# Kernel tuning notes

Measured on AMD Instinct MI355X. Metric: run time of the kernel, lower is better.

## Reference

```python
import jax, jax.numpy as jnp
import numpy as np

B, I, K, C = 4, 512, 512, 64
EPS_LN = 1e-5


def _ln_last2(x):
    # functional layer_norm over the last TWO dims, no affine params
    mu = x.mean(axis=(-2, -1), keepdims=True)
    var = ((x - mu) ** 2).mean(axis=(-2, -1), keepdims=True)
    return (x - mu) / jnp.sqrt(var + EPS_LN)


def setup_inputs() -> dict:
    key = jax.random.key(0)
    k1, k2, k3, k4, k5, k6, k7, k8 = jax.random.split(key, 8)
    V = jax.random.normal(k1, (B, I, C), dtype=jnp.float32)
    Q = jax.random.normal(k2, (B, K, C), dtype=jnp.float32)
    z = jax.random.normal(k3, (B, I, K, C), dtype=jnp.float32)
    z_mask = (jax.random.uniform(k4, (B, I, K)) > 0.3).astype(jnp.float32)
    s = 1.0 / np.sqrt(C)
    W1 = jax.random.normal(k5, (C, C), dtype=jnp.float32) * s
    b1 = jax.random.normal(k6, (C,), dtype=jnp.float32) * 0.01
    W2 = jax.random.normal(k7, (C, C), dtype=jnp.float32) * s
    b2 = jax.random.normal(k8, (C,), dtype=jnp.float32) * 0.01
    return {"V": V, "Q": Q, "z": z, "z_mask": z_mask,
            "W1": W1, "b1": b1, "W2": W2, "b2": b2, "dim": 1}


def reference(V, Q, z, z_mask, W1, b1, W2, b2, dim):
    normalize = True
    # masked exponential normalization along `dim` (per channel c)
    exp_z = jnp.exp(z) * (z_mask[..., None] + 1e-6)          # [b,i,k,c]
    zn = exp_z / exp_z.sum(axis=dim, keepdims=True)
    zn = z_mask[..., None] * zn
    Qa = Q @ W1.T + b1                                       # linear1
    if dim == 1:
        Va = jnp.einsum('bikc,bkc->bic', zn, Qa)
    else:
        Va = jnp.einsum('bikc,bic->bkc', zn, Qa)
    if normalize:
        Va = _ln_last2(Va)
    Vout = V + (Va @ W2.T + b2)                              # linear2 + residual
    if normalize:
        Vout = _ln_last2(Vout)
    return Vout
```

## Files before the change

kernel.cpp:

```cpp
#include <hip/hip_runtime.h>

constexpr int NB = 4;
constexpr int NI = 512;
constexpr int NK = 512;
constexpr int NC = 64;
constexpr float LN_EPS = 1e-5f;

__global__ __launch_bounds__(256) void k_S(const float* __restrict__ z,
                                           const float* __restrict__ zmask,
                                           float* __restrict__ S) {
    int idx = blockIdx.x;
    int ic = idx & 7;  idx >>= 3;
    int kt = idx & 31; int b = idx >> 5;
    int tid = threadIdx.x;
    int kk = tid >> 4;
    int c4 = tid & 15;
    int k = kt * 16 + kk;

    float4 acc = make_float4(0.f, 0.f, 0.f, 0.f);
    for (int ii = 0; ii < NI / 8; ++ii) {
        int i = ic * (NI / 8) + ii;
        size_t row = ((size_t)(b * NI + i) * NK + k) * NC;
        const float4 zv = *(const float4*)(z + row + c4 * 4);
        float m = zmask[(size_t)(b * NI + i) * NK + k] + 1e-6f;
        acc.x += __expf(zv.x) * m;
        acc.y += __expf(zv.y) * m;
        acc.z += __expf(zv.z) * m;
        acc.w += __expf(zv.w) * m;
    }
    float* sp = S + (size_t)(b * NK + k) * NC + c4 * 4;
    atomicAdd(sp + 0, acc.x);
    atomicAdd(sp + 1, acc.y);
    atomicAdd(sp + 2, acc.z);
    atomicAdd(sp + 3, acc.w);
}

__global__ __launch_bounds__(64) void k_R(const float* __restrict__ Q,
                                          const float* __restrict__ W1,
                                          const float* __restrict__ b1,
                                          const float* __restrict__ S,
                                          float* __restrict__ R) {
    int bk = blockIdx.x;
    int c = threadIdx.x;
    __shared__ float q[NC];
    q[c] = Q[(size_t)bk * NC + c];
    __syncthreads();
    const float* w = W1 + c * NC;
    float acc = b1[c];
#pragma unroll
    for (int j = 0; j < NC; ++j) acc += q[j] * w[j];
    R[(size_t)bk * NC + c] = acc / S[(size_t)bk * NC + c];
}

__global__ __launch_bounds__(256) void k_Va(const float* __restrict__ z,
                                            const float* __restrict__ zmask,
                                            const float* __restrict__ R,
                                            float* __restrict__ Va,
                                            float* __restrict__ part1) {
    int bi = blockIdx.x;
    int b = bi >> 9;
    int tid = threadIdx.x;
    int kk = tid >> 4;
    int c4 = tid & 15;

    const float* zrow = z + (size_t)bi * NK * NC;
    const float* mrow = zmask + (size_t)bi * NK;
    const float* Rb = R + (size_t)b * NK * NC;

    float4 acc = make_float4(0.f, 0.f, 0.f, 0.f);
    for (int kb = 0; kb < NK / 16; ++kb) {
        int k = kb * 16 + kk;
        const float4 zv = *(const float4*)(zrow + (size_t)k * NC + c4 * 4);
        const float4 rv = *(const float4*)(Rb + (size_t)k * NC + c4 * 4);
        float zm = mrow[k];
        float m2 = zm * (zm + 1e-6f);
        acc.x += __expf(zv.x) * m2 * rv.x;
        acc.y += __expf(zv.y) * m2 * rv.y;
        acc.z += __expf(zv.z) * m2 * rv.z;
        acc.w += __expf(zv.w) * m2 * rv.w;
    }

    __shared__ float4 part[256];
    part[tid] = acc;
    __syncthreads();
    for (int s = 128; s >= 16; s >>= 1) {
        if (tid < s) {
            float4 o = part[tid + s];
            float4 m = part[tid];
            m.x += o.x; m.y += o.y; m.z += o.z; m.w += o.w;
            part[tid] = m;
        }
        __syncthreads();
    }
    __shared__ float red[32];
    if (tid < 16) {
        float4 v = part[tid];
        *(float4*)(Va + (size_t)bi * NC + tid * 4) = v;
        red[tid]      = v.x + v.y + v.z + v.w;
        red[16 + tid] = v.x * v.x + v.y * v.y + v.z * v.z + v.w * v.w;
    }
    __syncthreads();
    if (tid == 0) {
        float s0 = 0.f, s1 = 0.f;
        for (int t = 0; t < 16; ++t) { s0 += red[t]; s1 += red[16 + t]; }
        part1[bi * 2]     = s0;
        part1[bi * 2 + 1] = s1;
    }
}

__global__ __launch_bounds__(256) void k_red(const float* __restrict__ part,
                                             float* __restrict__ stats) {
    int b = blockIdx.x;
    int tid = threadIdx.x;
    float s0 = 0.f, s1 = 0.f;
    for (int i = tid; i < NI; i += 256) {
        int bi = b * NI + i;
        s0 += part[bi * 2];
        s1 += part[bi * 2 + 1];
    }
    __shared__ float l0[256], l1[256];
    l0[tid] = s0; l1[tid] = s1;
    __syncthreads();
    for (int s = 128; s; s >>= 1) {
        if (tid < s) { l0[tid] += l0[tid + s]; l1[tid] += l1[tid + s]; }
        __syncthreads();
    }
    if (tid == 0) { stats[b * 2] = l0[0]; stats[b * 2 + 1] = l1[0]; }
}

__global__ __launch_bounds__(64) void k_Y(const float* __restrict__ V,
                                          const float* __restrict__ W2,
                                          const float* __restrict__ b2,
                                          const float* __restrict__ Va,
                                          const float* __restrict__ stats1,
                                          float* __restrict__ Y,
                                          float* __restrict__ part2) {
    int bi = blockIdx.x;
    int b = bi >> 9;
    int c = threadIdx.x;
    const float n = (float)(NI * NC);
    float mu = stats1[b * 2] / n;
    float var = stats1[b * 2 + 1] / n - mu * mu;
    float rstd = rsqrtf(var + LN_EPS);

    __shared__ float xn[NC];
    xn[c] = (Va[(size_t)bi * NC + c] - mu) * rstd;
    __syncthreads();

    const float* w = W2 + c * NC;
    float acc = b2[c];
#pragma unroll
    for (int j = 0; j < NC; ++j) acc += xn[j] * w[j];
    float y = V[(size_t)bi * NC + c] + acc;
    Y[(size_t)bi * NC + c] = y;

    float s0 = y, s1 = y * y;
    for (int off = 32; off; off >>= 1) {
        s0 += __shfl_down(s0, off);
        s1 += __shfl_down(s1, off);
    }
    if (c == 0) { part2[bi * 2] = s0; part2[bi * 2 + 1] = s1; }
}

__global__ __launch_bounds__(256) void k_out(const float* __restrict__ Y,
                                             const float* __restrict__ stats2,
                                             float* __restrict__ out) {
    int idx = blockIdx.x * 256 + threadIdx.x;
    int b = idx >> 15;
    const float n = (float)(NI * NC);
    float mu = stats2[b * 2] / n;
    float var = stats2[b * 2 + 1] / n - mu * mu;
    float rstd = rsqrtf(var + LN_EPS);
    out[idx] = (Y[idx] - mu) * rstd;
}

extern "C" void kernel_launch(void* const* d_in, const int* in_sizes, int n_in,
                              void* d_out, int out_size, void* d_ws, size_t ws_size,
                              hipStream_t stream) {
    const float* V  = (const float*)d_in[0];
    const float* Q  = (const float*)d_in[1];
    const float* z  = (const float*)d_in[2];
    const float* zm = (const float*)d_in[3];
    const float* W1 = (const float*)d_in[4];
    const float* b1 = (const float*)d_in[5];
    const float* W2 = (const float*)d_in[6];
    const float* b2 = (const float*)d_in[7];

    float* ws     = (float*)d_ws;
    float* S      = ws;
    float* R      = ws + 131072;
    float* Va     = ws + 262144;
    float* Y      = ws + 393216;
    float* part1  = ws + 524288;
    float* part2  = ws + 528384;
    float* stats1 = ws + 532480;
    float* stats2 = ws + 532488;

    hipMemsetAsync(S, 0, 131072 * sizeof(float), stream);

    k_S  <<<NB * (NK / 16) * 8, 256, 0, stream>>>(z, zm, S);
    k_R  <<<NB * NK,            64,  0, stream>>>(Q, W1, b1, S, R);
    k_Va <<<NB * NI,            256, 0, stream>>>(z, zm, R, Va, part1);
    k_red<<<NB,                 256, 0, stream>>>(part1, stats1);
    k_Y  <<<NB * NI,            64,  0, stream>>>(V, W2, b2, Va, stats1, Y, part2);
    k_red<<<NB,                 256, 0, stream>>>(part2, stats2);
    k_out<<<(NB * NI * NC) / 256, 256, 0, stream>>>(Y, stats2, (float*)d_out);
}
```

Baseline: 438.6 us.

## Process batches sequentially so z slice stays cached between sum and weighting passes

Splits the normalization-sum, R and weighted-accumulation kernels into a per-batch loop so the second read of each batch's z slice can hit the last-level cache instead of HBM. Replaces atomic accumulation into S (and its memset) with per-chunk partial sums written to workspace and reduced in k_R, using 32 i-chunks. Adds unroll pragmas. Trades more kernel launches and partial-sum traffic for halving expected DRAM reads of z.

```diff
diff --git a/kernel.cpp b/kernel.cpp
--- a/kernel.cpp
+++ b/kernel.cpp
@@ -6,20 +6,24 @@
 constexpr int NC = 64;
 constexpr float LN_EPS = 1e-5f;
 
+constexpr int IC = 32;
+constexpr int ILEN = NI / IC;
+
 __global__ __launch_bounds__(256) void k_S(const float* __restrict__ z,
                                            const float* __restrict__ zmask,
-                                           float* __restrict__ S) {
+                                           float* __restrict__ Spart, int b) {
     int idx = blockIdx.x;
-    int ic = idx & 7;  idx >>= 3;
-    int kt = idx & 31; int b = idx >> 5;
+    int ic = idx & (IC - 1);
+    int kt = idx >> 5;
     int tid = threadIdx.x;
     int kk = tid >> 4;
     int c4 = tid & 15;
     int k = kt * 16 + kk;
 
     float4 acc = make_float4(0.f, 0.f, 0.f, 0.f);
-    for (int ii = 0; ii < NI / 8; ++ii) {
-        int i = ic * (NI / 8) + ii;
+#pragma unroll 4
+    for (int ii = 0; ii < ILEN; ++ii) {
+        int i = ic * ILEN + ii;
         size_t row = ((size_t)(b * NI + i) * NK + k) * NC;
         const float4 zv = *(const float4*)(z + row + c4 * 4);
         float m = zmask[(size_t)(b * NI + i) * NK + k] + 1e-6f;
@@ -28,37 +32,37 @@
         acc.z += __expf(zv.z) * m;
         acc.w += __expf(zv.w) * m;
     }
-    float* sp = S + (size_t)(b * NK + k) * NC + c4 * 4;
-    atomicAdd(sp + 0, acc.x);
-    atomicAdd(sp + 1, acc.y);
-    atomicAdd(sp + 2, acc.z);
-    atomicAdd(sp + 3, acc.w);
+    *(float4*)(Spart + (size_t)ic * (NK * NC) + (size_t)k * NC + c4 * 4) = acc;
 }
 
 __global__ __launch_bounds__(64) void k_R(const float* __restrict__ Q,
                                           const float* __restrict__ W1,
                                           const float* __restrict__ b1,
-                                          const float* __restrict__ S,
-                                          float* __restrict__ R) {
-    int bk = blockIdx.x;
+                                          const float* __restrict__ Spart,
+                                          float* __restrict__ R, int b) {
+    int k = blockIdx.x;
     int c = threadIdx.x;
     __shared__ float q[NC];
-    q[c] = Q[(size_t)bk * NC + c];
+    q[c] = Q[((size_t)(b * NK) + k) * NC + c];
     __syncthreads();
     const float* w = W1 + c * NC;
     float acc = b1[c];
 #pragma unroll
     for (int j = 0; j < NC; ++j) acc += q[j] * w[j];
-    R[(size_t)bk * NC + c] = acc / S[(size_t)bk * NC + c];
+    float s = 0.f;
+#pragma unroll
+    for (int ic = 0; ic < IC; ++ic)
+        s += Spart[(size_t)ic * (NK * NC) + (size_t)k * NC + c];
+    R[((size_t)(b * NK) + k) * NC + c] = acc / s;
 }
 
 __global__ __launch_bounds__(256) void k_Va(const float* __restrict__ z,
                                             const float* __restrict__ zmask,
                                             const float* __restrict__ R,
                                             float* __restrict__ Va,
-                                            float* __restrict__ part1) {
-    int bi = blockIdx.x;
-    int b = bi >> 9;
+                                            float* __restrict__ part1, int b) {
+    int i = blockIdx.x;
+    int bi = b * NI + i;
     int tid = threadIdx.x;
     int kk = tid >> 4;
     int c4 = tid & 15;
@@ -68,6 +72,7 @@
     const float* Rb = R + (size_t)b * NK * NC;
 
     float4 acc = make_float4(0.f, 0.f, 0.f, 0.f);
+#pragma unroll 2
     for (int kb = 0; kb < NK / 16; ++kb) {
         int k = kb * 16 + kk;
         const float4 zv = *(const float4*)(zrow + (size_t)k * NC + c4 * 4);
@@ -187,20 +192,20 @@
     const float* b2 = (const float*)d_in[7];
 
     float* ws     = (float*)d_ws;
-    float* S      = ws;
-    float* R      = ws + 131072;
-    float* Va     = ws + 262144;
-    float* Y      = ws + 393216;
-    float* part1  = ws + 524288;
-    float* part2  = ws + 528384;
-    float* stats1 = ws + 532480;
-    float* stats2 = ws + 532488;
-
-    hipMemsetAsync(S, 0, 131072 * sizeof(float), stream);
-
-    k_S  <<<NB * (NK / 16) * 8, 256, 0, stream>>>(z, zm, S);
-    k_R  <<<NB * NK,            64,  0, stream>>>(Q, W1, b1, S, R);
-    k_Va <<<NB * NI,            256, 0, stream>>>(z, zm, R, Va, part1);
+    float* Spart  = ws;
+    float* R      = ws + 1048576;
+    float* Va     = ws + 1179648;
+    float* Y      = ws + 1310720;
+    float* part1  = ws + 1441792;
+    float* part2  = ws + 1445888;
+    float* stats1 = ws + 1449984;
+    float* stats2 = ws + 1449992;
+
+    for (int b = 0; b < NB; ++b) {
+        k_S <<<(NK / 16) * IC, 256, 0, stream>>>(z, zm, Spart, b);
+        k_R <<<NK,             64,  0, stream>>>(Q, W1, b1, Spart, R, b);
+        k_Va<<<NI,             256, 0, stream>>>(z, zm, R, Va, part1, b);
+    }
     k_red<<<NB,                 256, 0, stream>>>(part1, stats1);
     k_Y  <<<NB * NI,            64,  0, stream>>>(V, W2, b2, Va, stats1, Y, part2);
     k_red<<<NB,                 256, 0, stream>>>(part2, stats2);
```

Result: slower. 457.5 us (+4.3%).

## Replace atomic column sums with partial buffers and unroll z streaming loops

Applied to the files above, without the earlier changes.

The column-sum kernel now splits I into 16 chunks and writes per-chunk partial sums to a workspace buffer instead of using atomicAdd. The R kernel reduces those partials, which also removes the memset. Both z-streaming kernels are unrolled with four independent accumulators so more loads are in flight. This uses more workspace and adds extra partial-sum reads in k_R.

```diff
diff --git a/kernel.cpp b/kernel.cpp
--- a/kernel.cpp
+++ b/kernel.cpp
@@ -6,39 +6,57 @@
 constexpr int NC = 64;
 constexpr float LN_EPS = 1e-5f;
 
+constexpr int IC = 16;
+constexpr int ILEN = NI / IC;
+constexpr size_t SP_STRIDE = (size_t)NB * NK * NC;
+
 __global__ __launch_bounds__(256) void k_S(const float* __restrict__ z,
                                            const float* __restrict__ zmask,
-                                           float* __restrict__ S) {
+                                           float* __restrict__ Spart) {
     int idx = blockIdx.x;
-    int ic = idx & 7;  idx >>= 3;
+    int ic = idx & (IC - 1); idx >>= 4;
     int kt = idx & 31; int b = idx >> 5;
     int tid = threadIdx.x;
     int kk = tid >> 4;
     int c4 = tid & 15;
     int k = kt * 16 + kk;
 
-    float4 acc = make_float4(0.f, 0.f, 0.f, 0.f);
-    for (int ii = 0; ii < NI / 8; ++ii) {
-        int i = ic * (NI / 8) + ii;
-        size_t row = ((size_t)(b * NI + i) * NK + k) * NC;
-        const float4 zv = *(const float4*)(z + row + c4 * 4);
-        float m = zmask[(size_t)(b * NI + i) * NK + k] + 1e-6f;
-        acc.x += __expf(zv.x) * m;
-        acc.y += __expf(zv.y) * m;
-        acc.z += __expf(zv.z) * m;
-        acc.w += __expf(zv.w) * m;
-    }
-    float* sp = S + (size_t)(b * NK + k) * NC + c4 * 4;
-    atomicAdd(sp + 0, acc.x);
-    atomicAdd(sp + 1, acc.y);
-    atomicAdd(sp + 2, acc.z);
-    atomicAdd(sp + 3, acc.w);
+    float4 a0 = make_float4(0.f, 0.f, 0.f, 0.f);
+    float4 a1 = a0, a2 = a0, a3 = a0;
+
+    int i0 = ic * ILEN;
+#pragma unroll 2
+    for (int ii = 0; ii < ILEN; ii += 4) {
+        size_t base = (size_t)(b * NI + i0 + ii) * NK + k;
+        const float4 z0 = *(const float4*)(z + (base         ) * NC + c4 * 4);
+        const float4 z1 = *(const float4*)(z + (base +     NK) * NC + c4 * 4);
+        const float4 z2 = *(const float4*)(z + (base + 2 * NK) * NC + c4 * 4);
+        const float4 z3 = *(const float4*)(z + (base + 3 * NK) * NC + c4 * 4);
+        float m0 = zmask[base         ] + 1e-6f;
+        float m1 = zmask[base +     NK] + 1e-6f;
+        float m2 = zmask[base + 2 * NK] + 1e-6f;
+        float m3 = zmask[base + 3 * NK] + 1e-6f;
+        a0.x += __expf(z0.x) * m0; a0.y += __expf(z0.y) * m0;
+        a0.z += __expf(z0.z) * m0; a0.w += __expf(z0.w) * m0;
+        a1.x += __expf(z1.x) * m1; a1.y += __expf(z1.y) * m1;
+        a1.z += __expf(z1.z) * m1; a1.w += __expf(z1.w) * m1;
+        a2.x += __expf(z2.x) * m2; a2.y += __expf(z2.y) * m2;
+        a2.z += __expf(z2.z) * m2; a2.w += __expf(z2.w) * m2;
+        a3.x += __expf(z3.x) * m3; a3.y += __expf(z3.y) * m3;
+        a3.z += __expf(z3.z) * m3; a3.w += __expf(z3.w) * m3;
+    }
+    float4 acc;
+    acc.x = (a0.x + a1.x) + (a2.x + a3.x);
+    acc.y = (a0.y + a1.y) + (a2.y + a3.y);
+    acc.z = (a0.z + a1.z) + (a2.z + a3.z);
+    acc.w = (a0.w + a1.w) + (a2.w + a3.w);
+    *(float4*)(Spart + (size_t)ic * SP_STRIDE + ((size_t)(b * NK) + k) * NC + c4 * 4) = acc;
 }
 
 __global__ __launch_bounds__(64) void k_R(const float* __restrict__ Q,
                                           const float* __restrict__ W1,
                                           const float* __restrict__ b1,
-                                          const float* __restrict__ S,
+                                          const float* __restrict__ Spart,
                                           float* __restrict__ R) {
     int bk = blockIdx.x;
     int c = threadIdx.x;
@@ -49,7 +67,11 @@
     float acc = b1[c];
 #pragma unroll
     for (int j = 0; j < NC; ++j) acc += q[j] * w[j];
-    R[(size_t)bk * NC + c] = acc / S[(size_t)bk * NC + c];
+    float s = 0.f;
+#pragma unroll
+    for (int ic = 0; ic < IC; ++ic)
+        s += Spart[(size_t)ic * SP_STRIDE + (size_t)bk * NC + c];
+    R[(size_t)bk * NC + c] = acc / s;
 }
 
 __global__ __launch_bounds__(256) void k_Va(const float* __restrict__ z,
@@ -63,22 +85,41 @@
     int kk = tid >> 4;
     int c4 = tid & 15;
 
-    const float* zrow = z + (size_t)bi * NK * NC;
+    const float* zrow = z + (size_t)bi * NK * NC + c4 * 4;
     const float* mrow = zmask + (size_t)bi * NK;
-    const float* Rb = R + (size_t)b * NK * NC;
-
-    float4 acc = make_float4(0.f, 0.f, 0.f, 0.f);
-    for (int kb = 0; kb < NK / 16; ++kb) {
-        int k = kb * 16 + kk;
-        const float4 zv = *(const float4*)(zrow + (size_t)k * NC + c4 * 4);
-        const float4 rv = *(const float4*)(Rb + (size_t)k * NC + c4 * 4);
-        float zm = mrow[k];
-        float m2 = zm * (zm + 1e-6f);
-        acc.x += __expf(zv.x) * m2 * rv.x;
-        acc.y += __expf(zv.y) * m2 * rv.y;
-        acc.z += __expf(zv.z) * m2 * rv.z;
-        acc.w += __expf(zv.w) * m2 * rv.w;
-    }
+    const float* Rb = R + (size_t)b * NK * NC + c4 * 4;
+
+    float4 a0 = make_float4(0.f, 0.f, 0.f, 0.f);
+    float4 a1 = a0, a2 = a0, a3 = a0;
+#pragma unroll 2
+    for (int kb = 0; kb < NK / 64; ++kb) {
+        int k0 = kb * 64 + kk;
+        const float4 z0 = *(const float4*)(zrow + (size_t)(k0     ) * NC);
+        const float4 z1 = *(const float4*)(zrow + (size_t)(k0 + 16) * NC);
+        const float4 z2 = *(const float4*)(zrow + (size_t)(k0 + 32) * NC);
+        const float4 z3 = *(const float4*)(zrow + (size_t)(k0 + 48) * NC);
+        const float4 r0 = *(const float4*)(Rb + (size_t)(k0     ) * NC);
+        const float4 r1 = *(const float4*)(Rb + (size_t)(k0 + 16) * NC);
+        const float4 r2 = *(const float4*)(Rb + (size_t)(k0 + 32) * NC);
+        const float4 r3 = *(const float4*)(Rb + (size_t)(k0 + 48) * NC);
+        float w0 = mrow[k0];      w0 = w0 * (w0 + 1e-6f);
+        float w1 = mrow[k0 + 16]; w1 = w1 * (w1 + 1e-6f);
+        float w2 = mrow[k0 + 32]; w2 = w2 * (w2 + 1e-6f);
+        float w3 = mrow[k0 + 48]; w3 = w3 * (w3 + 1e-6f);
+        a0.x += __expf(z0.x) * w0 * r0.x; a0.y += __expf(z0.y) * w0 * r0.y;
+        a0.z += __expf(z0.z) * w0 * r0.z; a0.w += __expf(z0.w) * w0 * r0.w;
+        a1.x += __expf(z1.x) * w1 * r1.x; a1.y += __expf(z1.y) * w1 * r1.y;
+        a1.z += __expf(z1.z) * w1 * r1.z; a1.w += __expf(z1.w) * w1 * r1.w;
+        a2.x += __expf(z2.x) * w2 * r2.x; a2.y += __expf(z2.y) * w2 * r2.y;
+        a2.z += __expf(z2.z) * w2 * r2.z; a2.w += __expf(z2.w) * w2 * r2.w;
+        a3.x += __expf(z3.x) * w3 * r3.x; a3.y += __expf(z3.y) * w3 * r3.y;
+        a3.z += __expf(z3.z) * w3 * r3.z; a3.w += __expf(z3.w) * w3 * r3.w;
+    }
+    float4 acc;
+    acc.x = (a0.x + a1.x) + (a2.x + a3.x);
+    acc.y = (a0.y + a1.y) + (a2.y + a3.y);
+    acc.z = (a0.z + a1.z) + (a2.z + a3.z);
+    acc.w = (a0.w + a1.w) + (a2.w + a3.w);
 
     __shared__ float4 part[256];
     part[tid] = acc;
@@ -187,22 +228,20 @@
     const float* b2 = (const float*)d_in[7];
 
     float* ws     = (float*)d_ws;
-    float* S      = ws;
-    float* R      = ws + 131072;
-    float* Va     = ws + 262144;
-    float* Y      = ws + 393216;
-    float* part1  = ws + 524288;
-    float* part2  = ws + 528384;
-    float* stats1 = ws + 532480;
-    float* stats2 = ws + 532488;
-
-    hipMemsetAsync(S, 0, 131072 * sizeof(float), stream);
-
-    k_S  <<<NB * (NK / 16) * 8, 256, 0, stream>>>(z, zm, S);
-    k_R  <<<NB * NK,            64,  0, stream>>>(Q, W1, b1, S, R);
-    k_Va <<<NB * NI,            256, 0, stream>>>(z, zm, R, Va, part1);
-    k_red<<<NB,                 256, 0, stream>>>(part1, stats1);
-    k_Y  <<<NB * NI,            64,  0, stream>>>(V, W2, b2, Va, stats1, Y, part2);
-    k_red<<<NB,                 256, 0, stream>>>(part2, stats2);
+    float* Spart  = ws;
+    float* R      = ws + 2097152;
+    float* Va     = ws + 2228224;
+    float* Y      = ws + 2359296;
+    float* part1  = ws + 2490368;
+    float* part2  = ws + 2494464;
+    float* stats1 = ws + 2498560;
+    float* stats2 = ws + 2498568;
+
+    k_S  <<<NB * (NK / 16) * IC, 256, 0, stream>>>(z, zm, Spart);
+    k_R  <<<NB * NK,             64,  0, stream>>>(Q, W1, b1, Spart, R);
+    k_Va <<<NB * NI,             256, 0, stream>>>(z, zm, R, Va, part1);
+    k_red<<<NB,                  256, 0, stream>>>(part1, stats1);
+    k_Y  <<<NB * NI,             64,  0, stream>>>(V, W2, b2, Va, stats1, Y, part2);
+    k_red<<<NB,                  256, 0, stream>>>(part2, stats2);
     k_out<<<(NB * NI * NC) / 256, 256, 0, stream>>>(Y, stats2, (float*)d_out);
 }
```

Result: no change. 440.6 us (+0.5%).

## Stream contiguous z slabs per block and replace atomics with partial sums

Applied to the files above, without the earlier changes.

k_S now has each 512-thread block stream whole contiguous [K,C] slabs of z for a strided set of i rows. It keeps 16 float4 accumulators per thread and writes per-block partial S slabs instead of issuing atomicAdds, and the memset goes away. k_R sums the 64 partial slabs per (b,k,c). k_Va processes four full i-rows per block with the mask staged in LDS and uses a wave-shuffle reduction in place of the shared-memory tree. The aim is fully coalesced, contiguous reads of the 256MB z tensor and no atomic contention. The cost is a 32MB partial buffer, extra reads in k_R and higher register pressure in k_S.

```diff
diff --git a/kernel.cpp b/kernel.cpp
--- a/kernel.cpp
+++ b/kernel.cpp
@@ -6,41 +6,57 @@
 constexpr int NC = 64;
 constexpr float LN_EPS = 1e-5f;
 
-__global__ __launch_bounds__(256) void k_S(const float* __restrict__ z,
+
+constexpr int SBLK = 64;
+constexpr int SLAB = NK * NC;
+constexpr int NSLAB = NB * SBLK;
+
+__global__ __launch_bounds__(512) void k_S(const float* __restrict__ z,
                                            const float* __restrict__ zmask,
-                                           float* __restrict__ S) {
-    int idx = blockIdx.x;
-    int ic = idx & 7;  idx >>= 3;
-    int kt = idx & 31; int b = idx >> 5;
+                                           float* __restrict__ Spart) {
+    int blk = blockIdx.x;
+    int b = blk >> 6;
+    int ic = blk & (SBLK - 1);
     int tid = threadIdx.x;
-    int kk = tid >> 4;
-    int c4 = tid & 15;
-    int k = kt * 16 + kk;
-
-    float4 acc = make_float4(0.f, 0.f, 0.f, 0.f);
-    for (int ii = 0; ii < NI / 8; ++ii) {
-        int i = ic * (NI / 8) + ii;
-        size_t row = ((size_t)(b * NI + i) * NK + k) * NC;
-        const float4 zv = *(const float4*)(z + row + c4 * 4);
-        float m = zmask[(size_t)(b * NI + i) * NK + k] + 1e-6f;
-        acc.x += __expf(zv.x) * m;
-        acc.y += __expf(zv.y) * m;
-        acc.z += __expf(zv.z) * m;
-        acc.w += __expf(zv.w) * m;
-    }
-    float* sp = S + (size_t)(b * NK + k) * NC + c4 * 4;
-    atomicAdd(sp + 0, acc.x);
-    atomicAdd(sp + 1, acc.y);
-    atomicAdd(sp + 2, acc.z);
-    atomicAdd(sp + 3, acc.w);
+    int kg = tid >> 4;
+
+    __shared__ float mlds[NK];
+
+    float4 acc[16];
+#pragma unroll
+    for (int s = 0; s < 16; ++s) acc[s] = make_float4(0.f, 0.f, 0.f, 0.f);
+
+    for (int ii = 0; ii < NI / SBLK; ++ii) {
+        int i = ii * SBLK + ic;
+        const float* zs = z + (size_t)(b * NI + i) * SLAB;
+        const float* mp = zmask + (size_t)(b * NI + i) * NK;
+        __syncthreads();
+        mlds[tid] = mp[tid];
+        __syncthreads();
+#pragma unroll
+        for (int s = 0; s < 16; ++s) {
+            const float4 zv = *(const float4*)(zs + (size_t)(s * 512 + tid) * 4);
+            float w = mlds[s * 32 + kg] + 1e-6f;
+            acc[s].x += __expf(zv.x) * w;
+            acc[s].y += __expf(zv.y) * w;
+            acc[s].z += __expf(zv.z) * w;
+            acc[s].w += __expf(zv.w) * w;
+        }
+    }
+    float* sp = Spart + (size_t)blk * SLAB;
+#pragma unroll
+    for (int s = 0; s < 16; ++s)
+        *(float4*)(sp + (size_t)(s * 512 + tid) * 4) = acc[s];
 }
 
 __global__ __launch_bounds__(64) void k_R(const float* __restrict__ Q,
                                           const float* __restrict__ W1,
                                           const float* __restrict__ b1,
-                                          const float* __restrict__ S,
+                                          const float* __restrict__ Spart,
                                           float* __restrict__ R) {
     int bk = blockIdx.x;
+    int b = bk >> 9;
+    int k = bk & (NK - 1);
     int c = threadIdx.x;
     __shared__ float q[NC];
     q[c] = Q[(size_t)bk * NC + c];
@@ -49,62 +65,80 @@
     float acc = b1[c];
 #pragma unroll
     for (int j = 0; j < NC; ++j) acc += q[j] * w[j];
-    R[(size_t)bk * NC + c] = acc / S[(size_t)bk * NC + c];
-}
-
-__global__ __launch_bounds__(256) void k_Va(const float* __restrict__ z,
+    float s = 0.f;
+#pragma unroll 8
+    for (int j = 0; j < SBLK; ++j)
+        s += Spart[(size_t)((b << 6) + j) * SLAB + (size_t)k * NC + c];
+    R[(size_t)bk * NC + c] = acc / s;
+}
+
+__global__ __launch_bounds__(512) void k_Va(const float* __restrict__ z,
                                             const float* __restrict__ zmask,
                                             const float* __restrict__ R,
                                             float* __restrict__ Va,
                                             float* __restrict__ part1) {
-    int bi = blockIdx.x;
-    int b = bi >> 9;
+    int blk = blockIdx.x;
+    int b = blk >> 7;
+    int ic = blk & 127;
     int tid = threadIdx.x;
-    int kk = tid >> 4;
-    int c4 = tid & 15;
-
-    const float* zrow = z + (size_t)bi * NK * NC;
-    const float* mrow = zmask + (size_t)bi * NK;
-    const float* Rb = R + (size_t)b * NK * NC;
-
-    float4 acc = make_float4(0.f, 0.f, 0.f, 0.f);
-    for (int kb = 0; kb < NK / 16; ++kb) {
-        int k = kb * 16 + kk;
-        const float4 zv = *(const float4*)(zrow + (size_t)k * NC + c4 * 4);
-        const float4 rv = *(const float4*)(Rb + (size_t)k * NC + c4 * 4);
-        float zm = mrow[k];
-        float m2 = zm * (zm + 1e-6f);
-        acc.x += __expf(zv.x) * m2 * rv.x;
-        acc.y += __expf(zv.y) * m2 * rv.y;
-        acc.z += __expf(zv.z) * m2 * rv.z;
-        acc.w += __expf(zv.w) * m2 * rv.w;
-    }
-
-    __shared__ float4 part[256];
-    part[tid] = acc;
-    __syncthreads();
-    for (int s = 128; s >= 16; s >>= 1) {
-        if (tid < s) {
-            float4 o = part[tid + s];
-            float4 m = part[tid];
-            m.x += o.x; m.y += o.y; m.z += o.z; m.w += o.w;
-            part[tid] = m;
-        }
-        __syncthreads();
-    }
-    __shared__ float red[32];
-    if (tid < 16) {
-        float4 v = part[tid];
-        *(float4*)(Va + (size_t)bi * NC + tid * 4) = v;
-        red[tid]      = v.x + v.y + v.z + v.w;
-        red[16 + tid] = v.x * v.x + v.y * v.y + v.z * v.z + v.w * v.w;
-    }
-    __syncthreads();
-    if (tid == 0) {
-        float s0 = 0.f, s1 = 0.f;
-        for (int t = 0; t < 16; ++t) { s0 += red[t]; s1 += red[16 + t]; }
-        part1[bi * 2]     = s0;
-        part1[bi * 2 + 1] = s1;
+    int wave = tid >> 6;
+    int lane = tid & 63;
+    int kg = tid >> 4;
+
+    __shared__ float m2lds[NK];
+    __shared__ float4 wpart[8 * 16];
+
+    const float* Rb = R + (size_t)b * SLAB;
+
+    for (int ii = 0; ii < 4; ++ii) {
+        int i = ii * 128 + ic;
+        int bi = b * NI + i;
+        const float* zs = z + (size_t)bi * SLAB;
+        const float* mp = zmask + (size_t)bi * NK;
+        __syncthreads();
+        {
+            float m = mp[tid];
+            m2lds[tid] = m * (m + 1e-6f);
+        }
+        __syncthreads();
+
+        float4 a = make_float4(0.f, 0.f, 0.f, 0.f);
+#pragma unroll
+        for (int s = 0; s < 16; ++s) {
+            const float4 zv = *(const float4*)(zs + (size_t)(s * 512 + tid) * 4);
+            const float4 rv = *(const float4*)(Rb + (size_t)(s * 512 + tid) * 4);
+            float w = m2lds[s * 32 + kg];
+            a.x += __expf(zv.x) * w * rv.x;
+            a.y += __expf(zv.y) * w * rv.y;
+            a.z += __expf(zv.z) * w * rv.z;
+            a.w += __expf(zv.w) * w * rv.w;
+        }
+        a.x += __shfl_xor(a.x, 16); a.y += __shfl_xor(a.y, 16);
+        a.z += __shfl_xor(a.z, 16); a.w += __shfl_xor(a.w, 16);
+        a.x += __shfl_xor(a.x, 32); a.y += __shfl_xor(a.y, 32);
+        a.z += __shfl_xor(a.z, 32); a.w += __shfl_xor(a.w, 32);
+        if (lane < 16) wpart[wave * 16 + lane] = a;
+        __syncthreads();
+        if (tid < 16) {
+            float4 f = wpart[tid];
+#pragma unroll
+            for (int w = 1; w < 8; ++w) {
+                float4 o = wpart[w * 16 + tid];
+                f.x += o.x; f.y += o.y; f.z += o.z; f.w += o.w;
+            }
+            *(float4*)(Va + (size_t)bi * NC + tid * 4) = f;
+            float s0 = f.x + f.y + f.z + f.w;
+            float s1 = f.x * f.x + f.y * f.y + f.z * f.z + f.w * f.w;
+#pragma unroll
+            for (int off = 1; off < 16; off <<= 1) {
+                s0 += __shfl_xor(s0, off);
+                s1 += __shfl_xor(s1, off);
+            }
+            if (tid == 0) {
+                part1[bi * 2]     = s0;
+                part1[bi * 2 + 1] = s1;
+            }
+        }
     }
 }
 
@@ -187,22 +221,20 @@
     const float* b2 = (const float*)d_in[7];
 
     float* ws     = (float*)d_ws;
-    float* S      = ws;
-    float* R      = ws + 131072;
-    float* Va     = ws + 262144;
-    float* Y      = ws + 393216;
-    float* part1  = ws + 524288;
-    float* part2  = ws + 528384;
-    float* stats1 = ws + 532480;
-    float* stats2 = ws + 532488;
-
-    hipMemsetAsync(S, 0, 131072 * sizeof(float), stream);
-
-    k_S  <<<NB * (NK / 16) * 8, 256, 0, stream>>>(z, zm, S);
-    k_R  <<<NB * NK,            64,  0, stream>>>(Q, W1, b1, S, R);
-    k_Va <<<NB * NI,            256, 0, stream>>>(z, zm, R, Va, part1);
-    k_red<<<NB,                 256, 0, stream>>>(part1, stats1);
-    k_Y  <<<NB * NI,            64,  0, stream>>>(V, W2, b2, Va, stats1, Y, part2);
-    k_red<<<NB,                 256, 0, stream>>>(part2, stats2);
+    float* Spart  = ws;
+    float* R      = ws + 8388608;
+    float* Va     = ws + 8519680;
+    float* Y      = ws + 8650752;
+    float* part1  = ws + 8781824;
+    float* part2  = ws + 8785920;
+    float* stats1 = ws + 8790016;
+    float* stats2 = ws + 8790024;
+
+    k_S  <<<NSLAB,               512, 0, stream>>>(z, zm, Spart);
+    k_R  <<<NB * NK,             64,  0, stream>>>(Q, W1, b1, Spart, R);
+    k_Va <<<NB * 128,            512, 0, stream>>>(z, zm, R, Va, part1);
+    k_red<<<NB,                  256, 0, stream>>>(part1, stats1);
+    k_Y  <<<NB * NI,             64,  0, stream>>>(V, W2, b2, Va, stats1, Y, part2);
+    k_red<<<NB,                  256, 0, stream>>>(part2, stats2);
     k_out<<<(NB * NI * NC) / 256, 256, 0, stream>>>(Y, stats2, (float*)d_out);
 }
```

Result: slower. 454.3 us (+3.6%).
